# Performance work log

Measured on AMD Instinct MI355X. Metric: run time of the kernel, lower is better.

The kernel has to match this reference:

```python
import jax, jax.numpy as jnp
import numpy as np

B = 16            # number of graphs
IN_DIM, HID, OUT = 16, 64, 32
SIZES = np.array([256 + 16 * g for g in range(B)], dtype=np.int64)  # ragged graph sizes
N_TOT = int(SIZES.sum())            # 6016 nodes total
N_MAX = int(SIZES.max())            # 496
N_PAIRS = int((SIZES ** 2).sum())   # 2349056 valid (i,j) pairs


def setup_inputs() -> dict:
    key = jax.random.key(0)
    k_ape, k_w1, k_w2 = jax.random.split(key, 3)
    ape = jax.random.normal(k_ape, (N_TOT, IN_DIM), dtype=jnp.float32)
    W1 = jax.random.normal(k_w1, (IN_DIM, HID), dtype=jnp.float32) / np.sqrt(IN_DIM)
    b1 = jnp.zeros((HID,), dtype=jnp.float32)
    W2 = jax.random.normal(k_w2, (HID, OUT), dtype=jnp.float32) / np.sqrt(HID)
    b2 = jnp.zeros((OUT,), dtype=jnp.float32)
    batch = jnp.asarray(np.repeat(np.arange(B), SIZES), dtype=jnp.int32)
    return dict(ape=ape, W1=W1, b1=b1, W2=W2, b2=b2, batch=batch,
                num_graphs=B, n_max=N_MAX, n_pairs=N_PAIRS)


def reference(ape, W1, b1, W2, b2, batch, num_graphs, n_max, n_pairs):
    n_tot, in_dim = ape.shape
    # per-graph node counts and start offsets (equivalent of torch.bincount)
    counts = jax.ops.segment_sum(jnp.ones((n_tot,), jnp.int32), batch,
                                 num_segments=num_graphs)
    starts = jnp.cumsum(counts) - counts
    pos = jnp.arange(n_tot, dtype=jnp.int32) - starts[batch]
    # to_dense_batch: scatter ragged nodes into [B, n_max, in_dim] padded tensor
    dense = jnp.zeros((num_graphs, n_max, in_dim), ape.dtype).at[batch, pos].set(ape)
    # MLP: Linear -> ReLU -> Linear  (applied on padded dense batch as in the original)
    t = jax.nn.relu(dense @ W1 + b1) @ W2 + b2          # [B, n_max, OUT]
    # pairwise outer-sum: rpe[b,i,j] = t[b,i] + t[b,j]
    rpe = t[:, :, None, :] + t[:, None, :, :]           # [B, n_max, n_max, OUT]
    # from_dense_adj: gather valid (i<n_b, j<n_b) entries back to ragged layout
    node_mask = jnp.arange(n_max)[None, :] < counts[:, None]      # [B, n_max]
    pair_mask = node_mask[:, :, None] & node_mask[:, None, :]     # [B, n_max, n_max]
    bi, ii, jj = jnp.nonzero(pair_mask, size=n_pairs)             # static size -> jit-safe
    return rpe[bi, ii, jj]                                        # [n_pairs, OUT]
```

## Files before the change

### kernel.cpp

```cpp
#include <hip/hip_runtime.h>

#define IN_DIM   16
#define HID      64
#define OUT      32
#define NGRAPH   16
#define N_TOT    6016
#define N_PAIRS  2349056
#define TOTAL_F4 (N_PAIRS * (OUT / 4))

__host__ __device__ constexpr unsigned sumsq(unsigned n) {
    return n * (n + 1u) * (2u * n + 1u) / 6u;
}
__host__ __device__ constexpr unsigned poff_of(unsigned g) {
    return 256u * (sumsq(g + 15u) - 1240u);
}
static_assert(poff_of(3)  == 222464u,  "poff check");
static_assert(poff_of(15) == 2103040u, "poff check");
static_assert(poff_of(15) + 496u * 496u == (unsigned)N_PAIRS, "total check");

__global__ __launch_bounds__(256) void mlp_kernel(
    const float* __restrict__ ape, const float* __restrict__ W1,
    const float* __restrict__ b1,  const float* __restrict__ W2,
    const float* __restrict__ b2,  float* __restrict__ T)
{
    __shared__ float Hs[8][HID];
    __shared__ float W2s[HID * OUT];

    for (int idx = threadIdx.x; idx < HID * OUT; idx += 256)
        W2s[idx] = W2[idx];

    const int nl   = threadIdx.x >> 5;
    const int c    = threadIdx.x & 31;
    const int node = blockIdx.x * 8 + nl;

    float acc0 = b1[c];
    float acc1 = b1[c + 32];
    const float* a = ape + node * IN_DIM;
#pragma unroll
    for (int d = 0; d < IN_DIM; ++d) {
        const float av = a[d];
        acc0 += av * W1[d * HID + c];
        acc1 += av * W1[d * HID + c + 32];
    }
    Hs[nl][c]      = fmaxf(acc0, 0.0f);
    Hs[nl][c + 32] = fmaxf(acc1, 0.0f);
    __syncthreads();

    float t = b2[c];
#pragma unroll
    for (int k = 0; k < HID; ++k)
        t += Hs[nl][k] * W2s[k * OUT + c];
    T[node * OUT + c] = t;
}

__global__ __launch_bounds__(256) void pair_kernel(
    const float4* __restrict__ T4, float4* __restrict__ out4)
{
    const unsigned q = blockIdx.x * 256u + threadIdx.x;
    if (q >= (unsigned)TOTAL_F4) return;

    const unsigned p  = q >> 3;
    const unsigned c4 = q & 7;

    unsigned g = 0;
#pragma unroll
    for (unsigned k = 1; k < NGRAPH; ++k)
        g += (p >= poff_of(k)) ? 1u : 0u;

    const unsigned poffg = poff_of(g);
    const unsigned n     = 256u + (g << 4);
    const unsigned start = (g * (g + 31u)) << 3;

    const unsigned lp = p - poffg;
    const unsigned i  = (lp >> 4) / (g + 16u);
    const unsigned j  = lp - i * n;

    const float4 va = T4[(start + i) * (OUT / 4) + c4];
    const float4 vb = T4[(start + j) * (OUT / 4) + c4];
    out4[q] = make_float4(va.x + vb.x, va.y + vb.y, va.z + vb.z, va.w + vb.w);
}

extern "C" void kernel_launch(void* const* d_in, const int* in_sizes, int n_in,
                              void* d_out, int out_size, void* d_ws, size_t ws_size,
                              hipStream_t stream) {
    const float* ape = (const float*)d_in[0];
    const float* W1  = (const float*)d_in[1];
    const float* b1  = (const float*)d_in[2];
    const float* W2  = (const float*)d_in[3];
    const float* b2  = (const float*)d_in[4];

    float* T = (float*)d_ws;

    mlp_kernel<<<N_TOT / 8, 256, 0, stream>>>(ape, W1, b1, W2, b2, T);
    pair_kernel<<<TOTAL_F4 / 256, 256, 0, stream>>>((const float4*)T,
                                                    (float4*)d_out);
}
```

Baseline: 307.0 us.

## Restructure pair kernel to one block per output row with nontemporal stores

Replaces the flat per-float4 pair kernel with one block per node (output row). Each block finds its graph once, loads its own row vector, and loops over the j columns, which removes the per-element graph search and integer division. Output stores use nontemporal hints so the roughly 300 MB write stream bypasses cache. The trade-off is fixed-size blocks doing a variable number of loop iterations (8 to 16 per thread).

```diff
diff --git a/kernel.cpp b/kernel.cpp
--- a/kernel.cpp
+++ b/kernel.cpp
@@ -6,7 +6,8 @@
 #define NGRAPH   16
 #define N_TOT    6016
 #define N_PAIRS  2349056
-#define TOTAL_F4 (N_PAIRS * (OUT / 4))
+
+typedef float f4 __attribute__((ext_vector_type(4)));
 
 __host__ __device__ constexpr unsigned sumsq(unsigned n) {
     return n * (n + 1u) * (2u * n + 1u) / 6u;
@@ -14,9 +15,13 @@
 __host__ __device__ constexpr unsigned poff_of(unsigned g) {
     return 256u * (sumsq(g + 15u) - 1240u);
 }
+__host__ __device__ constexpr unsigned start_of(unsigned g) {
+    return 8u * g * (g + 31u);
+}
 static_assert(poff_of(3)  == 222464u,  "poff check");
 static_assert(poff_of(15) == 2103040u, "poff check");
 static_assert(poff_of(15) + 496u * 496u == (unsigned)N_PAIRS, "total check");
+static_assert(start_of(15) + 496u == (unsigned)N_TOT, "node total check");
 
 __global__ __launch_bounds__(256) void mlp_kernel(
     const float* __restrict__ ape, const float* __restrict__ W1,
@@ -53,31 +58,32 @@
     T[node * OUT + c] = t;
 }
 
-__global__ __launch_bounds__(256) void pair_kernel(
-    const float4* __restrict__ T4, float4* __restrict__ out4)
+__global__ __launch_bounds__(256) void pair_row_kernel(
+    const f4* __restrict__ T4, f4* __restrict__ out4)
 {
-    const unsigned q = blockIdx.x * 256u + threadIdx.x;
-    if (q >= (unsigned)TOTAL_F4) return;
-
-    const unsigned p  = q >> 3;
-    const unsigned c4 = q & 7;
+    const unsigned node = blockIdx.x;
 
     unsigned g = 0;
 #pragma unroll
     for (unsigned k = 1; k < NGRAPH; ++k)
-        g += (p >= poff_of(k)) ? 1u : 0u;
+        g += (node >= start_of(k)) ? 1u : 0u;
 
-    const unsigned poffg = poff_of(g);
-    const unsigned n     = 256u + (g << 4);
-    const unsigned start = (g * (g + 31u)) << 3;
+    const unsigned startg  = start_of(g);
+    const unsigned n       = 256u + (g << 4);
+    const unsigned i       = node - startg;
+    const unsigned rowbase = poff_of(g) + i * n;
 
-    const unsigned lp = p - poffg;
-    const unsigned i  = (lp >> 4) / (g + 16u);
-    const unsigned j  = lp - i * n;
+    const unsigned c4 = threadIdx.x & 7u;
+    const unsigned j0 = threadIdx.x >> 3;
 
-    const float4 va = T4[(start + i) * (OUT / 4) + c4];
-    const float4 vb = T4[(start + j) * (OUT / 4) + c4];
-    out4[q] = make_float4(va.x + vb.x, va.y + vb.y, va.z + vb.z, va.w + vb.w);
+    const f4 va = T4[node * 8u + c4];
+    const f4* __restrict__ tb = T4   + (size_t)startg  * 8u + c4;
+    f4* __restrict__       ob = out4 + (size_t)rowbase * 8u + c4;
+
+    for (unsigned j = j0; j < n; j += 32u) {
+        f4 v = va + tb[(size_t)j * 8u];
+        __builtin_nontemporal_store(v, &ob[(size_t)j * 8u]);
+    }
 }
 
 extern "C" void kernel_launch(void* const* d_in, const int* in_sizes, int n_in,
@@ -92,6 +98,5 @@
     float* T = (float*)d_ws;
 
     mlp_kernel<<<N_TOT / 8, 256, 0, stream>>>(ape, W1, b1, W2, b2, T);
-    pair_kernel<<<TOTAL_F4 / 256, 256, 0, stream>>>((const float4*)T,
-                                                    (float4*)d_out);
+    pair_row_kernel<<<N_TOT, 256, 0, stream>>>((const f4*)T, (f4*)d_out);
 }
```

Result: slower. 318.5 us (+3.7%).
